# Performance work log

Hardware: AMD Instinct MI355X
Metric: run time of the kernel (lower is better)

The kernel has to match this reference:

```python
import jax, jax.numpy as jnp
import numpy as np

NUM_CLASSES = 43
IMG_SIZE = 640.0
ALPHA, GAMMA = 0.25, 2.0
EPS = 1e-07


def _focal_loss(pred, target):
    p = jnp.clip(pred, EPS, 1.0 - EPS)
    pos = (target > 0.5).astype(p.dtype)
    neg = (target <= 0.5).astype(p.dtype)
    pos_loss = -ALPHA * (1.0 - p) ** GAMMA * jnp.log(p) * pos * target
    neg_loss = -(1.0 - ALPHA) * p ** GAMMA * jnp.log(1.0 - p) * neg * (1.0 - target)
    num_pos = jnp.maximum(pos.sum(), 1.0)
    return (pos_loss + neg_loss).sum() / num_pos


def _generate_targets(bboxes, labels, h, w):
    # bboxes: [B, M, 4] x1y1x2y2 in pixels; labels: [B, M] int (-1 = pad)
    B, M = labels.shape
    stride = IMG_SIZE / h
    x1, y1, x2, y2 = [bboxes[..., i] for i in range(4)]
    cx, cy = (x1 + x2) / 2.0, (y1 + y2) / 2.0
    bw, bh = x2 - x1, y2 - y1
    valid = (labels >= 0) & (bboxes.sum(-1) > 0) & (bw > 0) & (bh > 0)  # [B, M]

    gx = jnp.clip((cx / stride).astype(jnp.int32), 0, w - 1)
    gy = jnp.clip((cy / stride).astype(jnp.int32), 0, h - 1)
    # radius = sqrt(bw*bh)/stride clamped to >=2, then truncated to int
    r = jnp.maximum(jnp.sqrt(bw * bh) / stride, 2.0).astype(jnp.int32).astype(jnp.float32)
    sigma = r / 2.0

    gxf = gx.astype(jnp.float32)[:, :, None, None]  # [B,M,1,1]
    gyf = gy.astype(jnp.float32)[:, :, None, None]
    xg = jnp.arange(w, dtype=jnp.float32)[None, None, None, :]
    yg = jnp.arange(h, dtype=jnp.float32)[None, None, :, None]
    dist_sq = (xg - gxf) ** 2 + (yg - gyf) ** 2  # [B,M,H,W]
    r4 = r[:, :, None, None]
    s4 = sigma[:, :, None, None]
    gauss = jnp.exp(-dist_sq / (2.0 * s4 * s4))
    gauss = gauss * (dist_sq <= (2.0 * r4) ** 2) * valid[:, :, None, None]
    heatmap = gauss.max(axis=1)[:, None]  # [B,1,H,W]; max with implicit 0 init (gauss>=0)

    grid_cx = (gx.astype(jnp.float32) + 0.5) * stride
    grid_cy = (gy.astype(jnp.float32) + 0.5) * stride
    dx = (cx - grid_cx) / stride
    dy = (cy - grid_cy) / stride
    dw = jnp.log(bw / stride + 1e-06)
    dh = jnp.log(bh / stride + 1e-06)

    b_idx = jnp.broadcast_to(jnp.arange(B)[:, None], (B, M))
    gy_s = jnp.where(valid, gy, h)  # out-of-bounds -> dropped
    lab_s = jnp.clip(labels, 0, NUM_CLASSES - 1)

    box_targets = jnp.zeros((B, 4, h, w), jnp.float32)
    box_targets = box_targets.at[b_idx, 0, gy_s, gx].set(dx, mode='drop')
    box_targets = box_targets.at[b_idx, 1, gy_s, gx].set(dy, mode='drop')
    box_targets = box_targets.at[b_idx, 2, gy_s, gx].set(dw, mode='drop')
    box_targets = box_targets.at[b_idx, 3, gy_s, gx].set(dh, mode='drop')
    class_targets = jnp.zeros((B, NUM_CLASSES, h, w), jnp.float32)
    class_targets = class_targets.at[b_idx, lab_s, gy_s, gx].set(1.0, mode='drop')
    mask = jnp.zeros((B, 1, h, w), jnp.float32)
    mask = mask.at[b_idx, 0, gy_s, gx].set(1.0, mode='drop')
    return heatmap, box_targets, class_targets, mask


def setup_inputs() -> dict:
    key = jax.random.key(0)
    k1, k2, k3, k4, k5, k6 = jax.random.split(key, 6)
    B, M, H, W = 16, 64, 160, 160
    pred_heatmap = jax.random.uniform(k1, (B, 1, H, W), jnp.float32)
    pred_boxes = jax.random.normal(k2, (B, 4, H, W), jnp.float32)
    pred_classes = jax.random.normal(k3, (B, NUM_CLASSES, H, W), jnp.float32)
    pts = jax.random.uniform(k4, (B, M, 2, 2), jnp.float32) * IMG_SIZE  # two corners
    lo = jnp.min(pts, axis=2)
    hi = jnp.max(pts, axis=2) + 1.0
    bboxes = jnp.concatenate([lo, hi], axis=-1)  # x1,y1,x2,y2
    labels = jax.random.randint(k5, (B, M), 0, NUM_CLASSES)
    drop = jax.random.uniform(k6, (B, M)) < 0.3
    labels = jnp.where(drop, -1, labels).astype(jnp.int64)
    return {"pred_heatmap": pred_heatmap, "pred_boxes": pred_boxes,
            "pred_classes": pred_classes, "bboxes": bboxes, "labels": labels}


def reference(pred_heatmap, pred_boxes, pred_classes, bboxes, labels):
    B, _, h, w = pred_heatmap.shape
    t_heat, t_box, t_cls, mask = _generate_targets(bboxes, labels, h, w)
    heat_loss = _focal_loss(pred_heatmap, t_heat)
    num_pos = jnp.maximum(mask.sum(), 1.0)
    l1 = jnp.abs(pred_boxes * mask - t_box * mask).sum()
    box_loss = jnp.where(num_pos > 1, l1 / num_pos, 0.0)
    cmask = jnp.broadcast_to(mask, t_cls.shape)
    cls_raw = _focal_loss(jax.nn.sigmoid(pred_classes) * cmask, t_cls * cmask)
    cls_loss = jnp.where(num_pos > 1, cls_raw, 0.0)
    total = heat_loss + box_loss + cls_loss  # lambdas all 1.0
    return total
```

## Files before the change

kernel.cpp:

```cpp
#include <hip/hip_runtime.h>

#define HH 160
#define WW 160
#define HW (HH*WW)
#define NB 16
#define NM 64
#define NC 43
#define BLKX 50
#define NBLK (NB*BLKX)
#define CELLBASE NBLK

constexpr float STRIDE = 4.0f;
constexpr float EPSF = 1e-7f;
constexpr float BIGF = 3.4e38f;

__device__ __forceinline__ void box_geom(const float* __restrict__ bb,
                                         const int* __restrict__ labels, int tid,
                                         bool& valid, int& gx, int& gy,
                                         float& cx, float& cy, float& bw, float& bh) {
  float x1 = bb[tid * 4 + 0], y1 = bb[tid * 4 + 1];
  float x2 = bb[tid * 4 + 2], y2 = bb[tid * 4 + 3];
  cx = (x1 + x2) * 0.5f;
  cy = (y1 + y2) * 0.5f;
  bw = x2 - x1;
  bh = y2 - y1;
  int lab = labels[tid];
  valid = (lab >= 0) && ((x1 + y1 + x2 + y2) > 0.0f) && (bw > 0.0f) && (bh > 0.0f);
  int tgx = (int)(cx * 0.25f);
  int tgy = (int)(cy * 0.25f);
  gx = tgx < 0 ? 0 : (tgx > WW - 1 ? WW - 1 : tgx);
  gy = tgy < 0 ? 0 : (tgy > HH - 1 ? HH - 1 : tgy);
}

__global__ __launch_bounds__(128) void k_fused(const float* __restrict__ pred_heat,
                                               const float* __restrict__ pred_boxes,
                                               const float* __restrict__ pred_classes,
                                               const float* __restrict__ bboxes,
                                               const int* __restrict__ labels,
                                               float2* __restrict__ part) {
  __shared__ float4 sp[NM];
  __shared__ float lred[2];
  __shared__ int nred[2];

  int b = blockIdx.y, bx = blockIdx.x;
  int tid = threadIdx.x;
  int wave = tid >> 6, lane = tid & 63;

  if (tid < NM) {
    int t = b * NM + tid;
    bool valid; int gx, gy; float cx, cy, bw, bh;
    box_geom(bboxes, labels, t, valid, gx, gy, cx, cy, bw, bh);
    float rf = fmaxf(sqrtf(bw * bh) * 0.25f, 2.0f);
    float r = (float)(int)rf;
    float z = 2.0f / (r * r);
    float gxf = (float)gx, gyf = (float)gy;
    float4 p;
    p.x = z;
    p.y = -2.0f * z * gxf;
    p.z = -2.0f * z * gyf;
    p.w = valid ? z * fmaf(gxf, gxf, gyf * gyf) : __int_as_float(0x7fc00000);
    sp[tid] = p;
  }
  __syncthreads();

  int pixbase = bx * 512 + tid * 4;
  int idx = b * HW + pixbase;
  float4 pr4 = *(const float4*)(pred_heat + idx);
  int row = pixbase / WW;
  float xf0 = (float)(pixbase - row * WW);
  float yf = (float)row;
  float xf1 = xf0 + 1.0f, xf2 = xf0 + 2.0f, xf3 = xf0 + 3.0f;
  float yy = yf * yf;
  float s0 = fmaf(xf0, xf0, yy), s1 = fmaf(xf1, xf1, yy);
  float s2 = fmaf(xf2, xf2, yy), s3 = fmaf(xf3, xf3, yy);

  float m0 = BIGF, m1 = BIGF, m2 = BIGF, m3 = BIGF;
  #pragma unroll
  for (int m = 0; m < NM; m += 2) {
    float4 c0 = sp[m], c1 = sp[m + 1];
    { float base = fmaf(c0.z, yf, c0.w);
      m0 = fminf(m0, fmaf(c0.x, s0, fmaf(c0.y, xf0, base)));
      m1 = fminf(m1, fmaf(c0.x, s1, fmaf(c0.y, xf1, base)));
      m2 = fminf(m2, fmaf(c0.x, s2, fmaf(c0.y, xf2, base)));
      m3 = fminf(m3, fmaf(c0.x, s3, fmaf(c0.y, xf3, base))); }
    { float base = fmaf(c1.z, yf, c1.w);
      m0 = fminf(m0, fmaf(c1.x, s0, fmaf(c1.y, xf0, base)));
      m1 = fminf(m1, fmaf(c1.x, s1, fmaf(c1.y, xf1, base)));
      m2 = fminf(m2, fmaf(c1.x, s2, fmaf(c1.y, xf2, base)));
      m3 = fminf(m3, fmaf(c1.x, s3, fmaf(c1.y, xf3, base))); }
  }

  float t0 = (m0 <= 8.0f) ? __expf(-m0) : 0.0f;
  float t1 = (m1 <= 8.0f) ? __expf(-m1) : 0.0f;
  float t2 = (m2 <= 8.0f) ? __expf(-m2) : 0.0f;
  float t3 = (m3 <= 8.0f) ? __expf(-m3) : 0.0f;
  float p0 = fminf(fmaxf(pr4.x, EPSF), 1.0f - EPSF);
  float p1 = fminf(fmaxf(pr4.y, EPSF), 1.0f - EPSF);
  float p2 = fminf(fmaxf(pr4.z, EPSF), 1.0f - EPSF);
  float p3 = fminf(fmaxf(pr4.w, EPSF), 1.0f - EPSF);
  float q0 = 1.0f - p0, q1 = 1.0f - p1, q2 = 1.0f - p2, q3 = 1.0f - p3;
  bool o0 = t0 > 0.5f, o1 = t1 > 0.5f, o2 = t2 > 0.5f, o3 = t3 > 0.5f;
  float lg0 = __logf(o0 ? p0 : q0), lg1 = __logf(o1 ? p1 : q1);
  float lg2 = __logf(o2 ? p2 : q2), lg3 = __logf(o3 ? p3 : q3);
  float cf0 = o0 ? (-0.25f * q0 * q0 * t0) : (-0.75f * p0 * p0 * (1.0f - t0));
  float cf1 = o1 ? (-0.25f * q1 * q1 * t1) : (-0.75f * p1 * p1 * (1.0f - t1));
  float cf2 = o2 ? (-0.25f * q2 * q2 * t2) : (-0.75f * p2 * p2 * (1.0f - t2));
  float cf3 = o3 ? (-0.25f * q3 * q3 * t3) : (-0.75f * p3 * p3 * (1.0f - t3));
  float loss = fmaf(cf0, lg0, cf1 * lg1) + fmaf(cf2, lg2, cf3 * lg3);

  int cnt = __popcll(__ballot(o0)) + __popcll(__ballot(o1)) +
            __popcll(__ballot(o2)) + __popcll(__ballot(o3));
  #pragma unroll
  for (int off = 32; off > 0; off >>= 1) loss += __shfl_down(loss, off);
  if (lane == 0) { lred[wave] = loss; nred[wave] = cnt; }
  __syncthreads();
  if (tid == 0)
    part[b * BLKX + bx] = make_float2(lred[0] + lred[1], (float)(nred[0] + nred[1]));

  if (bx < 32) {
    int m = bx * 2 + wave;
    int lbox = b * NM + lane;
    bool valid; int gx, gy; float cx, cy, bw, bh;
    box_geom(bboxes, labels, lbox, valid, gx, gy, cx, cy, bw, bh);
    int lab = labels[lbox]; lab = lab < 0 ? 0 : (lab > NC - 1 ? NC - 1 : lab);

    int   valid_m = __shfl((int)valid, m);
    int   gx_m = __shfl(gx, m), gy_m = __shfl(gy, m);
    float cx_m = __shfl(cx, m), cy_m = __shfl(cy, m);
    float bw_m = __shfl(bw, m), bh_m = __shfl(bh, m);

    float l1 = 0.0f, csum = 0.0f;
    int cnt1 = 0, npos = 0;
    if (valid_m) {
      bool maps = valid && (gx == gx_m) && (gy == gy_m);
      unsigned long long mk = __ballot(maps);
      if ((63 - __clzll(mk)) == m) {
        unsigned long long cm = maps ? (1ull << lab) : 0ull;
        #pragma unroll
        for (int o = 1; o < 64; o <<= 1) cm |= __shfl_xor(cm, o);
        int celloff = gy_m * WW + gx_m;
        if (lane == 0) {
          float dxv = (cx_m - ((float)gx_m + 0.5f) * STRIDE) * 0.25f;
          float dyv = (cy_m - ((float)gy_m + 0.5f) * STRIDE) * 0.25f;
          float dwv = __logf(bw_m * 0.25f + 1e-6f);
          float dhv = __logf(bh_m * 0.25f + 1e-6f);
          const float* pb = pred_boxes + (size_t)b * 4 * HW + celloff;
          l1 = fabsf(pb[0] - dxv) + fabsf(pb[HW] - dyv) +
               fabsf(pb[2 * HW] - dwv) + fabsf(pb[3 * HW] - dhv);
          cnt1 = 1;
          npos = __popcll(cm);
        }
        if (lane < NC) {
          float x = pred_classes[(size_t)b * NC * HW + (size_t)lane * HW + celloff];
          float s = 1.0f / (1.0f + __expf(-x));
          float pc = fminf(fmaxf(s, EPSF), 1.0f - EPSF);
          float omc = 1.0f - pc;
          csum = ((cm >> lane) & 1ull) ? (-0.25f * omc * omc * __logf(pc))
                                       : (-0.75f * pc * pc * __logf(omc));
        }
        #pragma unroll
        for (int o = 32; o > 0; o >>= 1) csum += __shfl_down(csum, o);
      }
    }
    if (lane == 0) {
      int w = b * NM + m;
      part[CELLBASE + 2 * w]     = make_float2(l1, (float)cnt1);
      part[CELLBASE + 2 * w + 1] = make_float2(csum, (float)npos);
    }
  }
}

__global__ __launch_bounds__(256) void k_final(const float2* __restrict__ part,
                                               float* __restrict__ out) {
  int t = threadIdx.x;
  double hs = 0.0, hc = 0.0, l1 = 0.0, mc = 0.0, cs = 0.0, cp = 0.0;
  for (int i = t; i < NBLK; i += 256) {
    float2 v = part[i];
    hs += (double)v.x; hc += (double)v.y;
  }
  for (int i = t; i < NB * NM; i += 256) {
    float2 e0 = part[CELLBASE + 2 * i];
    float2 e1 = part[CELLBASE + 2 * i + 1];
    l1 += (double)e0.x; mc += (double)e0.y;
    cs += (double)e1.x; cp += (double)e1.y;
  }
  #pragma unroll
  for (int off = 32; off > 0; off >>= 1) {
    hs += __shfl_down(hs, off); hc += __shfl_down(hc, off);
    l1 += __shfl_down(l1, off); mc += __shfl_down(mc, off);
    cs += __shfl_down(cs, off); cp += __shfl_down(cp, off);
  }
  __shared__ double fin[4][6];
  int wave = t >> 6;
  if ((t & 63) == 0) {
    fin[wave][0] = hs; fin[wave][1] = hc; fin[wave][2] = l1;
    fin[wave][3] = mc; fin[wave][4] = cs; fin[wave][5] = cp;
  }
  __syncthreads();
  if (t == 0) {
    double HS = 0, HC = 0, L1 = 0, MC = 0, CS = 0, CP = 0;
    for (int i = 0; i < 4; ++i) {
      HS += fin[i][0]; HC += fin[i][1]; L1 += fin[i][2];
      MC += fin[i][3]; CS += fin[i][4]; CP += fin[i][5];
    }
    double nph = HC < 1.0 ? 1.0 : HC;
    float heat = (float)(HS / nph);
    float box = 0.0f, cls = 0.0f;
    if (MC > 1.5) {
      box = (float)(L1 / MC);
      double c = CP < 1.0 ? 1.0 : CP;
      cls = (float)(CS / c);
    }
    out[0] = heat + box + cls;
  }
}

extern "C" void kernel_launch(void* const* d_in, const int* in_sizes, int n_in,
                              void* d_out, int out_size, void* d_ws, size_t ws_size,
                              hipStream_t stream) {
  const float* pred_heat    = (const float*)d_in[0];
  const float* pred_boxes   = (const float*)d_in[1];
  const float* pred_classes = (const float*)d_in[2];
  const float* bboxes       = (const float*)d_in[3];
  const int*   labels       = (const int*)d_in[4];

  float2* part = (float2*)d_ws;

  dim3 grid(BLKX, NB);
  k_fused<<<grid, 128, 0, stream>>>(pred_heat, pred_boxes, pred_classes,
                                    bboxes, labels, part);
  k_final<<<1, 256, 0, stream>>>(part, (float*)d_out);
}
```

Measured before the change: 14.87 us.

## Fuse final reduction into main kernel via atomics and last-block ticket

Replaces the two-kernel partial-sum scheme with a single kernel. Each wave atomically adds its double-precision partials into per-batch accumulators, and the last block, chosen with a ticket counter, does the final reduction. Blocks grow from 128 to 256 threads and the grid halves. Box geometry is now loaded as a float4. A memset launch now zeroes the workspace, so the second kernel launch is traded for a memset plus contention on global double atomics.

```diff
diff --git a/kernel.cpp b/kernel.cpp
--- a/kernel.cpp
+++ b/kernel.cpp
@@ -6,41 +6,42 @@
 #define NB 16
 #define NM 64
 #define NC 43
-#define BLKX 50
+#define BLKX 25
 #define NBLK (NB*BLKX)
-#define CELLBASE NBLK
 
 constexpr float STRIDE = 4.0f;
 constexpr float EPSF = 1e-7f;
 constexpr float BIGF = 3.4e38f;
 
-__device__ __forceinline__ void box_geom(const float* __restrict__ bb,
-                                         const int* __restrict__ labels, int tid,
-                                         bool& valid, int& gx, int& gy,
-                                         float& cx, float& cy, float& bw, float& bh) {
-  float x1 = bb[tid * 4 + 0], y1 = bb[tid * 4 + 1];
-  float x2 = bb[tid * 4 + 2], y2 = bb[tid * 4 + 3];
-  cx = (x1 + x2) * 0.5f;
-  cy = (y1 + y2) * 0.5f;
-  bw = x2 - x1;
-  bh = y2 - y1;
-  int lab = labels[tid];
-  valid = (lab >= 0) && ((x1 + y1 + x2 + y2) > 0.0f) && (bw > 0.0f) && (bh > 0.0f);
+
+__device__ __forceinline__ void box_geom4(const float4* __restrict__ bb4,
+                                          const int* __restrict__ labels, int t,
+                                          bool& valid, int& gx, int& gy,
+                                          float& cx, float& cy, float& bw, float& bh) {
+  float4 v = bb4[t];
+  cx = (v.x + v.z) * 0.5f;
+  cy = (v.y + v.w) * 0.5f;
+  bw = v.z - v.x;
+  bh = v.w - v.y;
+  int lab = labels[t];
+  valid = (lab >= 0) && ((v.x + v.y + v.z + v.w) > 0.0f) && (bw > 0.0f) && (bh > 0.0f);
   int tgx = (int)(cx * 0.25f);
   int tgy = (int)(cy * 0.25f);
   gx = tgx < 0 ? 0 : (tgx > WW - 1 ? WW - 1 : tgx);
   gy = tgy < 0 ? 0 : (tgy > HH - 1 ? HH - 1 : tgy);
 }
 
-__global__ __launch_bounds__(128) void k_fused(const float* __restrict__ pred_heat,
-                                               const float* __restrict__ pred_boxes,
-                                               const float* __restrict__ pred_classes,
-                                               const float* __restrict__ bboxes,
-                                               const int* __restrict__ labels,
-                                               float2* __restrict__ part) {
+__global__ __launch_bounds__(256) void k_all(const float* __restrict__ pred_heat,
+                                             const float* __restrict__ pred_boxes,
+                                             const float* __restrict__ pred_classes,
+                                             const float4* __restrict__ bboxes,
+                                             const int* __restrict__ labels,
+                                             double* __restrict__ acc,
+                                             unsigned int* __restrict__ ticket,
+                                             float* __restrict__ out) {
   __shared__ float4 sp[NM];
-  __shared__ float lred[2];
-  __shared__ int nred[2];
+  __shared__ int islast;
+  __shared__ double fin[96];
 
   int b = blockIdx.y, bx = blockIdx.x;
   int tid = threadIdx.x;
@@ -49,7 +50,7 @@
   if (tid < NM) {
     int t = b * NM + tid;
     bool valid; int gx, gy; float cx, cy, bw, bh;
-    box_geom(bboxes, labels, t, valid, gx, gy, cx, cy, bw, bh);
+    box_geom4(bboxes, labels, t, valid, gx, gy, cx, cy, bw, bh);
     float rf = fmaxf(sqrtf(bw * bh) * 0.25f, 2.0f);
     float r = (float)(int)rf;
     float z = 2.0f / (r * r);
@@ -63,7 +64,7 @@
   }
   __syncthreads();
 
-  int pixbase = bx * 512 + tid * 4;
+  int pixbase = bx * 1024 + tid * 4;
   int idx = b * HW + pixbase;
   float4 pr4 = *(const float4*)(pred_heat + idx);
   int row = pixbase / WW;
@@ -112,16 +113,16 @@
             __popcll(__ballot(o2)) + __popcll(__ballot(o3));
   #pragma unroll
   for (int off = 32; off > 0; off >>= 1) loss += __shfl_down(loss, off);
-  if (lane == 0) { lred[wave] = loss; nred[wave] = cnt; }
-  __syncthreads();
-  if (tid == 0)
-    part[b * BLKX + bx] = make_float2(lred[0] + lred[1], (float)(nred[0] + nred[1]));
-
-  if (bx < 32) {
-    int m = bx * 2 + wave;
+  if (lane == 0) {
+    atomicAdd(&acc[0 * 16 + b], (double)loss);
+    atomicAdd(&acc[1 * 16 + b], (double)cnt);
+  }
+
+  if (bx < 16) {
+    int m = bx * 4 + wave;
     int lbox = b * NM + lane;
     bool valid; int gx, gy; float cx, cy, bw, bh;
-    box_geom(bboxes, labels, lbox, valid, gx, gy, cx, cy, bw, bh);
+    box_geom4(bboxes, labels, lbox, valid, gx, gy, cx, cy, bw, bh);
     int lab = labels[lbox]; lab = lab < 0 ? 0 : (lab > NC - 1 ? NC - 1 : lab);
 
     int   valid_m = __shfl((int)valid, m);
@@ -129,8 +130,6 @@
     float cx_m = __shfl(cx, m), cy_m = __shfl(cy, m);
     float bw_m = __shfl(bw, m), bh_m = __shfl(bh, m);
 
-    float l1 = 0.0f, csum = 0.0f;
-    int cnt1 = 0, npos = 0;
     if (valid_m) {
       bool maps = valid && (gx == gx_m) && (gy == gy_m);
       unsigned long long mk = __ballot(maps);
@@ -139,17 +138,7 @@
         #pragma unroll
         for (int o = 1; o < 64; o <<= 1) cm |= __shfl_xor(cm, o);
         int celloff = gy_m * WW + gx_m;
-        if (lane == 0) {
-          float dxv = (cx_m - ((float)gx_m + 0.5f) * STRIDE) * 0.25f;
-          float dyv = (cy_m - ((float)gy_m + 0.5f) * STRIDE) * 0.25f;
-          float dwv = __logf(bw_m * 0.25f + 1e-6f);
-          float dhv = __logf(bh_m * 0.25f + 1e-6f);
-          const float* pb = pred_boxes + (size_t)b * 4 * HW + celloff;
-          l1 = fabsf(pb[0] - dxv) + fabsf(pb[HW] - dyv) +
-               fabsf(pb[2 * HW] - dwv) + fabsf(pb[3 * HW] - dhv);
-          cnt1 = 1;
-          npos = __popcll(cm);
-        }
+        float csum = 0.0f;
         if (lane < NC) {
           float x = pred_classes[(size_t)b * NC * HW + (size_t)lane * HW + celloff];
           float s = 1.0f / (1.0f + __expf(-x));
@@ -160,48 +149,41 @@
         }
         #pragma unroll
         for (int o = 32; o > 0; o >>= 1) csum += __shfl_down(csum, o);
+        if (lane == 0) {
+          float dxv = (cx_m - ((float)gx_m + 0.5f) * STRIDE) * 0.25f;
+          float dyv = (cy_m - ((float)gy_m + 0.5f) * STRIDE) * 0.25f;
+          float dwv = __logf(bw_m * 0.25f + 1e-6f);
+          float dhv = __logf(bh_m * 0.25f + 1e-6f);
+          const float* pb = pred_boxes + (size_t)b * 4 * HW + celloff;
+          float l1 = fabsf(pb[0] - dxv) + fabsf(pb[HW] - dyv) +
+                     fabsf(pb[2 * HW] - dwv) + fabsf(pb[3 * HW] - dhv);
+          atomicAdd(&acc[2 * 16 + b], (double)l1);
+          atomicAdd(&acc[3 * 16 + b], 1.0);
+          atomicAdd(&acc[4 * 16 + b], (double)csum);
+          atomicAdd(&acc[5 * 16 + b], (double)__popcll(cm));
+        }
       }
     }
-    if (lane == 0) {
-      int w = b * NM + m;
-      part[CELLBASE + 2 * w]     = make_float2(l1, (float)cnt1);
-      part[CELLBASE + 2 * w + 1] = make_float2(csum, (float)npos);
-    }
-  }
-}
-
-__global__ __launch_bounds__(256) void k_final(const float2* __restrict__ part,
-                                               float* __restrict__ out) {
-  int t = threadIdx.x;
-  double hs = 0.0, hc = 0.0, l1 = 0.0, mc = 0.0, cs = 0.0, cp = 0.0;
-  for (int i = t; i < NBLK; i += 256) {
-    float2 v = part[i];
-    hs += (double)v.x; hc += (double)v.y;
-  }
-  for (int i = t; i < NB * NM; i += 256) {
-    float2 e0 = part[CELLBASE + 2 * i];
-    float2 e1 = part[CELLBASE + 2 * i + 1];
-    l1 += (double)e0.x; mc += (double)e0.y;
-    cs += (double)e1.x; cp += (double)e1.y;
-  }
-  #pragma unroll
-  for (int off = 32; off > 0; off >>= 1) {
-    hs += __shfl_down(hs, off); hc += __shfl_down(hc, off);
-    l1 += __shfl_down(l1, off); mc += __shfl_down(mc, off);
-    cs += __shfl_down(cs, off); cp += __shfl_down(cp, off);
-  }
-  __shared__ double fin[4][6];
-  int wave = t >> 6;
-  if ((t & 63) == 0) {
-    fin[wave][0] = hs; fin[wave][1] = hc; fin[wave][2] = l1;
-    fin[wave][3] = mc; fin[wave][4] = cs; fin[wave][5] = cp;
-  }
-  __syncthreads();
-  if (t == 0) {
+  }
+
+  asm volatile("s_waitcnt vmcnt(0)" ::: "memory");
+  __syncthreads();
+  if (tid == 0) {
+    unsigned int old = atomicAdd(ticket, 1u);
+    islast = (old == NBLK - 1) ? 1 : 0;
+  }
+  __syncthreads();
+  if (!islast) return;
+
+  if (tid < 96) fin[tid] = atomicAdd(&acc[tid], 0.0);
+  __syncthreads();
+  if (tid == 0) {
     double HS = 0, HC = 0, L1 = 0, MC = 0, CS = 0, CP = 0;
-    for (int i = 0; i < 4; ++i) {
-      HS += fin[i][0]; HC += fin[i][1]; L1 += fin[i][2];
-      MC += fin[i][3]; CS += fin[i][4]; CP += fin[i][5];
+    #pragma unroll
+    for (int i = 0; i < 16; ++i) {
+      HS += fin[i];      HC += fin[16 + i];
+      L1 += fin[32 + i]; MC += fin[48 + i];
+      CS += fin[64 + i]; CP += fin[80 + i];
     }
     double nph = HC < 1.0 ? 1.0 : HC;
     float heat = (float)(HS / nph);
@@ -218,16 +200,18 @@
 extern "C" void kernel_launch(void* const* d_in, const int* in_sizes, int n_in,
                               void* d_out, int out_size, void* d_ws, size_t ws_size,
                               hipStream_t stream) {
-  const float* pred_heat    = (const float*)d_in[0];
-  const float* pred_boxes   = (const float*)d_in[1];
-  const float* pred_classes = (const float*)d_in[2];
-  const float* bboxes       = (const float*)d_in[3];
-  const int*   labels       = (const int*)d_in[4];
-
-  float2* part = (float2*)d_ws;
-
+  const float*  pred_heat    = (const float*)d_in[0];
+  const float*  pred_boxes   = (const float*)d_in[1];
+  const float*  pred_classes = (const float*)d_in[2];
+  const float4* bboxes       = (const float4*)d_in[3];
+  const int*    labels       = (const int*)d_in[4];
+
+  char* ws = (char*)d_ws;
+  double* acc = (double*)ws;
+  unsigned int* ticket = (unsigned int*)(ws + 768);
+
+  hipMemsetAsync(ws, 0, 772, stream);
   dim3 grid(BLKX, NB);
-  k_fused<<<grid, 128, 0, stream>>>(pred_heat, pred_boxes, pred_classes,
-                                    bboxes, labels, part);
-  k_final<<<1, 256, 0, stream>>>(part, (float*)d_out);
+  k_all<<<grid, 256, 0, stream>>>(pred_heat, pred_boxes, pred_classes,
+                                  bboxes, labels, acc, ticket, (float*)d_out);
 }
```

Result: slower. 37.78 us (+154.0%).
